# Optimization experiments

Hardware: AMD Instinct MI355X
Metric: run time of the kernel (lower is better)

## Reference

```python
import jax, jax.numpy as jnp
import numpy as np

B, H, W = 8, 56, 56
DIM, DIM_OUT, NUM_HEADS = 96, 192, 3
Q_STRIDE = (2, 2)


def setup_inputs() -> dict:
    key = jax.random.key(0)
    k1, k2, k3 = jax.random.split(key, 3)
    x = jax.random.normal(k1, (B, H, W, DIM), dtype=jnp.float32)
    W_qkv = jax.random.normal(k2, (DIM, 3 * DIM_OUT), dtype=jnp.float32) * 0.02
    b_qkv = jnp.zeros((3 * DIM_OUT,), dtype=jnp.float32)
    W_proj = jax.random.normal(k3, (DIM_OUT, DIM_OUT), dtype=jnp.float32) * 0.02
    b_proj = jnp.zeros((DIM_OUT,), dtype=jnp.float32)
    return {"x": x, "W_qkv": W_qkv, "b_qkv": b_qkv, "W_proj": W_proj, "b_proj": b_proj}


def reference(x, W_qkv, b_qkv, W_proj, b_proj):
    b, h, w, _ = x.shape
    c = W_proj.shape[0]          # dim_out
    nh = NUM_HEADS
    hd = c // nh                 # head_dim
    sh, sw = Q_STRIDE

    # fused QKV projection: (B,H,W,3*C)
    qkv = jnp.einsum("bhwd,de->bhwe", x, W_qkv) + b_qkv
    qkv = qkv.reshape(b, h * w, 3, nh, hd)
    q, k, v = qkv[:, :, 0], qkv[:, :, 1], qkv[:, :, 2]  # each (B,N,nh,hd)

    # query max-pool over spatial dims (channels = nh*hd, heads interleaved as in original)
    q = q.reshape(b, h, w, c)
    q = q.reshape(b, h // sh, sh, w // sw, sw, c).max(axis=(2, 4))  # (B,H',W',C)
    hn, wn = h // sh, w // sw
    q = q.reshape(b, hn * wn, nh, hd)

    # heads-first layout, scaled q
    q = q.transpose(0, 2, 1, 3) / jnp.sqrt(jnp.asarray(hd, x.dtype))  # (B,nh,Nq,hd)
    k = k.transpose(0, 2, 1, 3)                                       # (B,nh,Nk,hd)
    v = v.transpose(0, 2, 1, 3)

    attn = jax.nn.softmax(jnp.einsum("bnqd,bnkd->bnqk", q, k), axis=-1)
    out = jnp.einsum("bnqk,bnkd->bnqd", attn, v)        # (B,nh,Nq,hd)
    out = out.transpose(0, 2, 1, 3).reshape(b, hn, wn, c)

    return jnp.einsum("bhwc,cd->bhwd", out, W_proj) + b_proj
```

## Files before the change

### kernel.cpp

```cpp
#include <hip/hip_runtime.h>

#define BB    8
#define DIMO  192
#define NH    3
#define HD    64
#define NK    3136
#define NQ    784
#define M1    25088
#define M2    6272
#define KSPLIT 7
#define KSLICE 448
#define PSTR  56

#define QSCALE 0.18033688011112042f

#if __has_builtin(__builtin_amdgcn_mfma_f32_16x16x16bf16_1k)
#define HAVE_MFMA16 1
#else
#define HAVE_MFMA16 0
#endif

#if __has_builtin(__builtin_amdgcn_exp2f)
#define FEXP2(x) __builtin_amdgcn_exp2f(x)
#else
#define FEXP2(x) exp2f(x)
#endif

typedef __bf16 bf16x8 __attribute__((ext_vector_type(8)));
typedef float f32x4  __attribute__((ext_vector_type(4)));
typedef short s16x4  __attribute__((ext_vector_type(4)));

__device__ inline unsigned short f2bf(float f) {
    unsigned int u = __builtin_bit_cast(unsigned int, f);
    u += 0x7FFFu + ((u >> 16) & 1u);
    return (unsigned short)(u >> 16);
}

__device__ inline unsigned int pk_bf16(float a, float b) {
    unsigned int ua = __builtin_bit_cast(unsigned int, a) + 0x8000u;
    unsigned int ub = __builtin_bit_cast(unsigned int, b) + 0x8000u;
    return __builtin_amdgcn_perm(ub, ua, 0x07060302u);
}

__global__ void wprep(const float* __restrict__ Wqkv, const float* __restrict__ Wproj,
                      unsigned short* __restrict__ Wb, unsigned short* __restrict__ Wpb) {
    __shared__ float Ls[192][33];
    const int t = threadIdx.x;
    if (blockIdx.x < 18) {
        const int n0 = blockIdx.x * 32;
        int rr = t >> 5, c = t & 31;
#pragma unroll
        for (int rb = 0; rb < 12; ++rb) {
            int row = rb * 8 + rr;
            Ls[row][c] = Wqkv[(size_t)row * 576 + n0 + c];
        }
        __syncthreads();
        int n = t >> 3, kc = (t & 7) * 12;
#pragma unroll
        for (int j = 0; j < 12; j += 4) {
            ushort4 u = { f2bf(Ls[kc + j][n]), f2bf(Ls[kc + j + 1][n]),
                          f2bf(Ls[kc + j + 2][n]), f2bf(Ls[kc + j + 3][n]) };
            *(ushort4*)(Wb + (size_t)(n0 + n) * 96 + kc + j) = u;
        }
    } else {
        const int n0 = (blockIdx.x - 18) * 32;
        int rr = t >> 5, c = t & 31;
#pragma unroll
        for (int rb = 0; rb < 24; ++rb) {
            int row = rb * 8 + rr;
            Ls[row][c] = Wproj[(size_t)row * 192 + n0 + c];
        }
        __syncthreads();
        int n = t >> 3, kc = (t & 7) * 24;
#pragma unroll
        for (int j = 0; j < 24; j += 4) {
            ushort4 u = { f2bf(Ls[kc + j][n]), f2bf(Ls[kc + j + 1][n]),
                          f2bf(Ls[kc + j + 2][n]), f2bf(Ls[kc + j + 3][n]) };
            *(ushort4*)(Wpb + (size_t)(n0 + n) * 192 + kc + j) = u;
        }
    }
}

__launch_bounds__(256)
__global__ void qkv_fused(const float* __restrict__ x,
                          const unsigned short* __restrict__ Wb,
                          const float* __restrict__ bias,
                          unsigned short* __restrict__ Qpb,
                          unsigned short* __restrict__ Kb,
                          unsigned short* __restrict__ Vt) {
    __shared__ __attribute__((aligned(16))) unsigned short xs[112 * 104];
    const int tid = threadIdx.x;
    const int wave = tid >> 6, lane = tid & 63;
    const int quad = lane >> 4, l16 = lane & 15;
    const int bid = blockIdx.x;

    if (bid < 392) {
        const int m0 = bid * 64;
#pragma unroll
        for (int i = 0; i < 6; ++i) {
            int f = tid + i * 256;
            int r = f / 24, c4 = f % 24;
            float4 v = ((const float4*)x)[(size_t)(m0 + r) * 24 + c4];
            ushort4 u = { f2bf(v.x), f2bf(v.y), f2bf(v.z), f2bf(v.w) };
            *(ushort4*)&xs[r * 104 + c4 * 4] = u;
        }
        __syncthreads();

        const int mbase = m0 + wave * 16 + quad * 4;
        const int b = m0 / NK;
        const int key = mbase - b * NK;

#pragma unroll
        for (int sec = 1; sec <= 2; ++sec) {
            f32x4 acc[12];
#pragma unroll
            for (int i = 0; i < 12; ++i) acc[i] = (f32x4){0.f, 0.f, 0.f, 0.f};

            const unsigned short* wb = Wb + (size_t)(sec * 192 + l16) * 96 + quad * 8;
#pragma unroll
            for (int ch = 0; ch < 3; ++ch) {
                bf16x8 af = *(const bf16x8*)&xs[(wave * 16 + l16) * 104 + ch * 32 + quad * 8];
#pragma unroll
                for (int nf = 0; nf < 12; ++nf) {
                    bf16x8 bfr = *(const bf16x8*)(wb + (size_t)nf * 16 * 96 + ch * 32);
                    acc[nf] = __builtin_amdgcn_mfma_f32_16x16x32_bf16(af, bfr, acc[nf], 0, 0, 0);
                }
            }

            if (sec == 1) {
#pragma unroll
                for (int nf = 0; nf < 12; ++nf) {
                    int n = nf * 16 + l16;
                    float bs = bias[192 + n];
#pragma unroll
                    for (int i = 0; i < 4; ++i)
                        Kb[(size_t)(mbase + i) * 192 + n] = f2bf(acc[nf][i] + bs);
                }
            } else {
#pragma unroll
                for (int nf = 0; nf < 12; ++nf) {
                    int n = nf * 16 + l16;
                    float bs = bias[384 + n];
                    int hh = n >> 6, dd = n & 63;
                    ushort4 u = { f2bf(acc[nf][0] + bs), f2bf(acc[nf][1] + bs),
                                  f2bf(acc[nf][2] + bs), f2bf(acc[nf][3] + bs) };
                    *(ushort4*)(Vt + ((size_t)((b * 3 + hh) * 64 + dd)) * NK + key) = u;
                }
            }
        }
    } else {
        const int t = bid - 392;
        const int b = t / 28, hq = t % 28;
        const int m0 = b * NK + hq * 112;
#pragma unroll
        for (int i = 0; i < 11; ++i) {
            int f = tid + i * 256;
            if (f < 2688) {
                int r = f / 24, c4 = f % 24;
                float4 v = ((const float4*)x)[(size_t)(m0 + r) * 24 + c4];
                int rp = 2 * (r % 56) + (r / 56);
                ushort4 u = { f2bf(v.x), f2bf(v.y), f2bf(v.z), f2bf(v.w) };
                *(ushort4*)&xs[rp * 104 + c4 * 4] = u;
            }
        }
        __syncthreads();

        f32x4 acc[7][3];
#pragma unroll
        for (int i = 0; i < 7; ++i)
#pragma unroll
            for (int j = 0; j < 3; ++j) acc[i][j] = (f32x4){0.f, 0.f, 0.f, 0.f};

        const unsigned short* wb = Wb + (size_t)(wave * 48 + l16) * 96 + quad * 8;
#pragma unroll
        for (int ch = 0; ch < 3; ++ch) {
            bf16x8 bfr[3];
#pragma unroll
            for (int jf = 0; jf < 3; ++jf)
                bfr[jf] = *(const bf16x8*)(wb + (size_t)jf * 16 * 96 + ch * 32);
#pragma unroll
            for (int mf = 0; mf < 7; ++mf) {
                bf16x8 a = *(const bf16x8*)&xs[(mf * 16 + l16) * 104 + ch * 32 + quad * 8];
#pragma unroll
                for (int jf = 0; jf < 3; ++jf)
                    acc[mf][jf] = __builtin_amdgcn_mfma_f32_16x16x32_bf16(a, bfr[jf], acc[mf][jf], 0, 0, 0);
            }
        }

#pragma unroll
        for (int mf = 0; mf < 7; ++mf) {
            int q = hq * 28 + mf * 4 + quad;
#pragma unroll
            for (int jf = 0; jf < 3; ++jf) {
                int n = wave * 48 + jf * 16 + l16;
                float m = fmaxf(fmaxf(acc[mf][jf][0], acc[mf][jf][1]),
                                fmaxf(acc[mf][jf][2], acc[mf][jf][3]));
                m = (m + bias[n]) * QSCALE;
                int hh = n >> 6, dd = n & 63;
                Qpb[((size_t)(b * 3 + hh) * NQ + q) * 64 + dd] = f2bf(m);
            }
        }
    }
}

__launch_bounds__(256)
__global__ void attn_mfma(const unsigned short* __restrict__ Qpb,
                          const unsigned short* __restrict__ Kb,
                          const unsigned short* __restrict__ Vt,
                          float* __restrict__ Pnum,
                          float* __restrict__ Pden) {
    __shared__ __attribute__((aligned(16))) unsigned short Ks[64 * 88];
    __shared__ __attribute__((aligned(16))) unsigned short Vs[64 * 88];
#if !HAVE_MFMA16
    __shared__ __attribute__((aligned(16))) unsigned short Ps[4 * 32 * PSTR];
#endif

    const int tid = threadIdx.x;
    const int wave = tid >> 6, lane = tid & 63;
    const int quad = lane >> 4, l16 = lane & 15;
    const int bh = blockIdx.y, b = bh / NH, h = bh % NH;
    const int qt = blockIdx.x * 128 + wave * 32;
    const int ks = blockIdx.z, k00 = ks * KSLICE;

    const int srow0 = tid >> 3, sch = (tid & 7) * 8;
    const unsigned short* kg  = Kb + ((size_t)(b * NK + k00) + srow0) * DIMO + h * 64 + sch;
    const unsigned short* kg1 = kg + (size_t)32 * DIMO;
    const unsigned short* vg  = Vt + ((size_t)bh * 64 + srow0) * NK + k00 + sch;
    const unsigned short* vg1 = vg + (size_t)32 * NK;

    uint4 kp0 = *(const uint4*)kg;
    uint4 kp1 = *(const uint4*)kg1;
    uint4 vp0 = *(const uint4*)vg;
    uint4 vp1 = *(const uint4*)vg1;

    int qa = min(qt + l16, NQ - 1);
    int qb = min(qt + 16 + l16, NQ - 1);
    const unsigned short* qpa = Qpb + ((size_t)bh * NQ + qa) * HD + quad * 8;
    const unsigned short* qpc = Qpb + ((size_t)bh * NQ + qb) * HD + quad * 8;
    bf16x8 qf[2][2];
    qf[0][0] = *(const bf16x8*)qpa;  qf[0][1] = *(const bf16x8*)(qpa + 32);
    qf[1][0] = *(const bf16x8*)qpc;  qf[1][1] = *(const bf16x8*)(qpc + 32);

    f32x4 on[4][2];
#pragma unroll
    for (int i = 0; i < 4; ++i)
#pragma unroll
        for (int j = 0; j < 2; ++j) on[i][j] = (f32x4){0.f, 0.f, 0.f, 0.f};
    f32x4 dn[2];
    dn[0] = (f32x4){0.f, 0.f, 0.f, 0.f};
    dn[1] = (f32x4){0.f, 0.f, 0.f, 0.f};

#if HAVE_MFMA16
    const short one16 = (short)0x3F80;
    s16x4 ones4 = { one16, one16, one16, one16 };
#else
    const __bf16 one = (__bf16)1.0f;
    bf16x8 ones8 = { one, one, one, one, one, one, one, one };
    unsigned short* myP = Ps + wave * 32 * PSTR;
#endif

    for (int s = 0; s < 7; ++s) {
        __syncthreads();
        *(uint4*)&Ks[srow0 * 88 + sch]        = kp0;
        *(uint4*)&Ks[(srow0 + 32) * 88 + sch] = kp1;
        *(uint4*)&Vs[srow0 * 88 + sch]        = vp0;
        *(uint4*)&Vs[(srow0 + 32) * 88 + sch] = vp1;
        __syncthreads();
        if (s < 6) {
            kp0 = *(const uint4*)(kg  + (size_t)(s + 1) * 64 * DIMO);
            kp1 = *(const uint4*)(kg1 + (size_t)(s + 1) * 64 * DIMO);
            vp0 = *(const uint4*)(vg  + (s + 1) * 64);
            vp1 = *(const uint4*)(vg1 + (s + 1) * 64);
        }

#if HAVE_MFMA16
#pragma unroll
        for (int g = 0; g < 4; ++g) {
            const int krow = (g * 16 + l16) * 88;
            bf16x8 kf0 = *(const bf16x8*)&Ks[krow + quad * 8];
            bf16x8 kf1 = *(const bf16x8*)&Ks[krow + 32 + quad * 8];
            s16x4 vf[4];
#pragma unroll
            for (int dsub = 0; dsub < 4; ++dsub)
                vf[dsub] = *(const s16x4*)&Vs[(dsub * 16 + l16) * 88 + g * 16 + quad * 4];
#pragma unroll
            for (int qsub = 0; qsub < 2; ++qsub) {
                f32x4 sa = (f32x4){0.f, 0.f, 0.f, 0.f};
                sa = __builtin_amdgcn_mfma_f32_16x16x32_bf16(kf0, qf[qsub][0], sa, 0, 0, 0);
                sa = __builtin_amdgcn_mfma_f32_16x16x32_bf16(kf1, qf[qsub][1], sa, 0, 0, 0);
                float p0 = FEXP2(sa[0]), p1 = FEXP2(sa[1]);
                float p2 = FEXP2(sa[2]), p3 = FEXP2(sa[3]);
                uint2 pk = { pk_bf16(p0, p1), pk_bf16(p2, p3) };
                s16x4 pb = __builtin_bit_cast(s16x4, pk);
                dn[qsub] = __builtin_amdgcn_mfma_f32_16x16x16bf16_1k(ones4, pb, dn[qsub], 0, 0, 0);
#pragma unroll
                for (int dsub = 0; dsub < 4; ++dsub)
                    on[dsub][qsub] = __builtin_amdgcn_mfma_f32_16x16x16bf16_1k(
                        vf[dsub], pb, on[dsub][qsub], 0, 0, 0);
            }
        }
#else
#pragma unroll
        for (int half = 0; half < 2; ++half) {
#pragma unroll
            for (int ksub = 0; ksub < 2; ++ksub) {
                const int krow = (half * 32 + ksub * 16 + l16) * 88;
                bf16x8 kf0 = *(const bf16x8*)&Ks[krow + quad * 8];
                bf16x8 kf1 = *(const bf16x8*)&Ks[krow + 32 + quad * 8];
#pragma unroll
                for (int qsub = 0; qsub < 2; ++qsub) {
                    f32x4 sa = (f32x4){0.f, 0.f, 0.f, 0.f};
                    sa = __builtin_amdgcn_mfma_f32_16x16x32_bf16(kf0, qf[qsub][0], sa, 0, 0, 0);
                    sa = __builtin_amdgcn_mfma_f32_16x16x32_bf16(kf1, qf[qsub][1], sa, 0, 0, 0);
                    float p0 = FEXP2(sa[0]), p1 = FEXP2(sa[1]);
                    float p2 = FEXP2(sa[2]), p3 = FEXP2(sa[3]);
                    uint2 pk = { pk_bf16(p0, p1), pk_bf16(p2, p3) };
                    *(uint2*)&myP[(qsub * 16 + l16) * PSTR + ksub * 16 + quad * 4] = pk;
                }
            }
            bf16x8 pf0 = *(const bf16x8*)&myP[l16 * PSTR + quad * 8];
            bf16x8 pf1 = *(const bf16x8*)&myP[(16 + l16) * PSTR + quad * 8];
            dn[0] = __builtin_amdgcn_mfma_f32_16x16x32_bf16(ones8, pf0, dn[0], 0, 0, 0);
            dn[1] = __builtin_amdgcn_mfma_f32_16x16x32_bf16(ones8, pf1, dn[1], 0, 0, 0);
#pragma unroll
            for (int dsub = 0; dsub < 4; ++dsub) {
                bf16x8 vf = *(const bf16x8*)&Vs[(dsub * 16 + l16) * 88 + half * 32 + quad * 8];
                on[dsub][0] = __builtin_amdgcn_mfma_f32_16x16x32_bf16(vf, pf0, on[dsub][0], 0, 0, 0);
                on[dsub][1] = __builtin_amdgcn_mfma_f32_16x16x32_bf16(vf, pf1, on[dsub][1], 0, 0, 0);
            }
        }
#endif
    }

#pragma unroll
    for (int qsub = 0; qsub < 2; ++qsub) {
        int q = qt + qsub * 16 + l16;
        if (q < NQ) {
            size_t base = (size_t)ks * (24 * NQ * HD) + ((size_t)bh * NQ + q) * HD + quad * 4;
#pragma unroll
            for (int dsub = 0; dsub < 4; ++dsub)
                *(f32x4*)(Pnum + base + dsub * 16) = on[dsub][qsub];
            if (quad == 0) Pden[ks * (24 * NQ) + bh * NQ + q] = dn[qsub][0];
        }
    }
}

__launch_bounds__(256)
__global__ void proj_comb(const float* __restrict__ Pnum,
                          const float* __restrict__ Pden,
                          const unsigned short* __restrict__ Wpb,
                          const float* __restrict__ bproj,
                          float* __restrict__ out) {
    __shared__ __attribute__((aligned(16))) unsigned short as_[16 * 200];
    __shared__ float rden[16][4];
    const int tid = threadIdx.x;
    const int wave = tid >> 6, lane = tid & 63;
    const int quad = lane >> 4, l16 = lane & 15;
    const int m0 = blockIdx.x * 16;

    if (tid < 48) {
        int r = tid / 3, h = tid % 3;
        int gq = m0 + r, b = gq / NQ, qq = gq - b * NQ;
        float den = 0.f;
#pragma unroll
        for (int s = 0; s < KSPLIT; ++s)
            den += Pden[s * (24 * NQ) + (b * 3 + h) * NQ + qq];
        rden[r][h] = 1.0f / den;
    }
    __syncthreads();

    {
        int r = tid >> 4, cl = tid & 15;
        int gq = m0 + r, b = gq / NQ, qq = gq - b * NQ;
#pragma unroll
        for (int i = 0; i < 3; ++i) {
            int c = cl + i * 16;
            int h = c >> 4, d = (c & 15) * 4;
            const float* p = Pnum + ((size_t)(b * 3 + h) * NQ + qq) * 64 + d;
            f32x4 num = (f32x4){0.f, 0.f, 0.f, 0.f};
#pragma unroll
            for (int s = 0; s < KSPLIT; ++s)
                num = num + *(const f32x4*)(p + (size_t)s * (24 * NQ * HD));
            float rc = rden[r][h];
            ushort4 u = { f2bf(num[0] * rc), f2bf(num[1] * rc),
                          f2bf(num[2] * rc), f2bf(num[3] * rc) };
            *(ushort4*)&as_[r * 200 + c * 4] = u;
        }
    }
    __syncthreads();

    f32x4 acc[3];
#pragma unroll
    for (int j = 0; j < 3; ++j) acc[j] = (f32x4){0.f, 0.f, 0.f, 0.f};

    const unsigned short* wp = Wpb + (size_t)(wave * 48 + l16) * 192 + quad * 8;
#pragma unroll
    for (int ch = 0; ch < 6; ++ch) {
        bf16x8 a = *(const bf16x8*)&as_[l16 * 200 + ch * 32 + quad * 8];
#pragma unroll
        for (int jf = 0; jf < 3; ++jf) {
            bf16x8 bfr = *(const bf16x8*)(wp + (size_t)jf * 16 * 192 + ch * 32);
            acc[jf] = __builtin_amdgcn_mfma_f32_16x16x32_bf16(a, bfr, acc[jf], 0, 0, 0);
        }
    }

    const int m = m0 + quad * 4;
#pragma unroll
    for (int jf = 0; jf < 3; ++jf) {
        int n = wave * 48 + jf * 16 + l16;
        float bs = bproj[n];
#pragma unroll
        for (int i = 0; i < 4; ++i)
            out[(size_t)(m + i) * 192 + n] = acc[jf][i] + bs;
    }
}

extern "C" void kernel_launch(void* const* d_in, const int* in_sizes, int n_in,
                              void* d_out, int out_size, void* d_ws, size_t ws_size,
                              hipStream_t stream) {
    const float* x     = (const float*)d_in[0];
    const float* Wqkv  = (const float*)d_in[1];
    const float* bqkv  = (const float*)d_in[2];
    const float* Wproj = (const float*)d_in[3];
    const float* bproj = (const float*)d_in[4];
    float* out = (float*)d_out;

    float* Pnum = (float*)d_ws;
    float* Pden = Pnum + (size_t)KSPLIT * 24 * NQ * HD;
    unsigned short* Qpb = (unsigned short*)(Pden + (size_t)KSPLIT * 24 * NQ);
    unsigned short* Kb  = Qpb + (size_t)24 * NQ * HD;
    unsigned short* Vt  = Kb + (size_t)BB * NK * DIMO;
    unsigned short* Wb  = Vt + (size_t)24 * HD * NK;
    unsigned short* Wpb = Wb + (size_t)576 * 96;

    wprep<<<24, 256, 0, stream>>>(Wqkv, Wproj, Wb, Wpb);

    qkv_fused<<<616, 256, 0, stream>>>(x, Wb, bqkv, Qpb, Kb, Vt);

    attn_mfma<<<dim3(7, 24, KSPLIT), 256, 0, stream>>>(Qpb, Kb, Vt, Pnum, Pden);

    proj_comb<<<392, 256, 0, stream>>>(Pnum, Pden, Wpb, bproj, out);
}
```

Baseline: 138.4 us.

## Split K/V blocks, remap attention grid per XCD, store partial numerators as bf16

```diff
diff --git a/kernel.cpp b/kernel.cpp
--- a/kernel.cpp
+++ b/kernel.cpp
@@ -34,6 +34,11 @@
     unsigned int u = __builtin_bit_cast(unsigned int, f);
     u += 0x7FFFu + ((u >> 16) & 1u);
     return (unsigned short)(u >> 16);
+}
+
+__device__ inline float bf2f(unsigned short u) {
+    unsigned int x = (unsigned int)u << 16;
+    return __builtin_bit_cast(float, x);
 }
 
 __device__ inline unsigned int pk_bf16(float a, float b) {
@@ -94,8 +99,9 @@
     const int quad = lane >> 4, l16 = lane & 15;
     const int bid = blockIdx.x;
 
-    if (bid < 392) {
-        const int m0 = bid * 64;
+    if (bid < 784) {
+        const int sec = (bid < 392) ? 1 : 2;
+        const int m0 = ((bid < 392) ? bid : bid - 392) * 64;
 #pragma unroll
         for (int i = 0; i < 6; ++i) {
             int f = tid + i * 256;
@@ -106,50 +112,46 @@
         }
         __syncthreads();
 
+        f32x4 acc[12];
+#pragma unroll
+        for (int i = 0; i < 12; ++i) acc[i] = (f32x4){0.f, 0.f, 0.f, 0.f};
+
+        const unsigned short* wb = Wb + (size_t)(sec * 192 + l16) * 96 + quad * 8;
+#pragma unroll
+        for (int ch = 0; ch < 3; ++ch) {
+            bf16x8 af = *(const bf16x8*)&xs[(wave * 16 + l16) * 104 + ch * 32 + quad * 8];
+#pragma unroll
+            for (int nf = 0; nf < 12; ++nf) {
+                bf16x8 bfr = *(const bf16x8*)(wb + (size_t)nf * 16 * 96 + ch * 32);
+                acc[nf] = __builtin_amdgcn_mfma_f32_16x16x32_bf16(af, bfr, acc[nf], 0, 0, 0);
+            }
+        }
+
         const int mbase = m0 + wave * 16 + quad * 4;
-        const int b = m0 / NK;
-        const int key = mbase - b * NK;
-
-#pragma unroll
-        for (int sec = 1; sec <= 2; ++sec) {
-            f32x4 acc[12];
-#pragma unroll
-            for (int i = 0; i < 12; ++i) acc[i] = (f32x4){0.f, 0.f, 0.f, 0.f};
-
-            const unsigned short* wb = Wb + (size_t)(sec * 192 + l16) * 96 + quad * 8;
-#pragma unroll
-            for (int ch = 0; ch < 3; ++ch) {
-                bf16x8 af = *(const bf16x8*)&xs[(wave * 16 + l16) * 104 + ch * 32 + quad * 8];
-#pragma unroll
-                for (int nf = 0; nf < 12; ++nf) {
-                    bf16x8 bfr = *(const bf16x8*)(wb + (size_t)nf * 16 * 96 + ch * 32);
-                    acc[nf] = __builtin_amdgcn_mfma_f32_16x16x32_bf16(af, bfr, acc[nf], 0, 0, 0);
-                }
-            }
-
-            if (sec == 1) {
-#pragma unroll
-                for (int nf = 0; nf < 12; ++nf) {
-                    int n = nf * 16 + l16;
-                    float bs = bias[192 + n];
-#pragma unroll
-                    for (int i = 0; i < 4; ++i)
-                        Kb[(size_t)(mbase + i) * 192 + n] = f2bf(acc[nf][i] + bs);
-                }
-            } else {
-#pragma unroll
-                for (int nf = 0; nf < 12; ++nf) {
-                    int n = nf * 16 + l16;
-                    float bs = bias[384 + n];
-                    int hh = n >> 6, dd = n & 63;
-                    ushort4 u = { f2bf(acc[nf][0] + bs), f2bf(acc[nf][1] + bs),
-                                  f2bf(acc[nf][2] + bs), f2bf(acc[nf][3] + bs) };
-                    *(ushort4*)(Vt + ((size_t)((b * 3 + hh) * 64 + dd)) * NK + key) = u;
-                }
+        if (sec == 1) {
+#pragma unroll
+            for (int nf = 0; nf < 12; ++nf) {
+                int n = nf * 16 + l16;
+                float bs = bias[192 + n];
+#pragma unroll
+                for (int i = 0; i < 4; ++i)
+                    Kb[(size_t)(mbase + i) * 192 + n] = f2bf(acc[nf][i] + bs);
+            }
+        } else {
+            int b = m0 / NK;
+            int key = mbase - b * NK;
+#pragma unroll
+            for (int nf = 0; nf < 12; ++nf) {
+                int n = nf * 16 + l16;
+                float bs = bias[384 + n];
+                int hh = n >> 6, dd = n & 63;
+                ushort4 u = { f2bf(acc[nf][0] + bs), f2bf(acc[nf][1] + bs),
+                              f2bf(acc[nf][2] + bs), f2bf(acc[nf][3] + bs) };
+                *(ushort4*)(Vt + ((size_t)((b * 3 + hh) * 64 + dd)) * NK + key) = u;
             }
         }
     } else {
-        const int t = bid - 392;
+        const int t = bid - 784;
         const int b = t / 28, hq = t % 28;
         const int m0 = b * NK + hq * 112;
 #pragma unroll
@@ -207,7 +209,7 @@
 __global__ void attn_mfma(const unsigned short* __restrict__ Qpb,
                           const unsigned short* __restrict__ Kb,
                           const unsigned short* __restrict__ Vt,
-                          float* __restrict__ Pnum,
+                          unsigned short* __restrict__ Pnum,
                           float* __restrict__ Pden) {
     __shared__ __attribute__((aligned(16))) unsigned short Ks[64 * 88];
     __shared__ __attribute__((aligned(16))) unsigned short Vs[64 * 88];
@@ -218,9 +220,16 @@
     const int tid = threadIdx.x;
     const int wave = tid >> 6, lane = tid & 63;
     const int quad = lane >> 4, l16 = lane & 15;
-    const int bh = blockIdx.y, b = bh / NH, h = bh % NH;
-    const int qt = blockIdx.x * 128 + wave * 32;
-    const int ks = blockIdx.z, k00 = ks * KSLICE;
+
+    const int bid = blockIdx.x;
+    const int xcd = bid & 7, slot = bid >> 3;
+    const int bh = xcd * 3 + slot / 49;
+    const int inner = slot % 49;
+    const int qt = (inner / 7) * 128 + wave * 32;
+    const int ks = inner % 7;
+
+    const int b = bh / NH, h = bh % NH;
+    const int k00 = ks * KSLICE;
 
     const int srow0 = tid >> 3, sch = (tid & 7) * 8;
     const unsigned short* kg  = Kb + ((size_t)(b * NK + k00) + srow0) * DIMO + h * 64 + sch;
@@ -338,15 +347,18 @@
         if (q < NQ) {
             size_t base = (size_t)ks * (24 * NQ * HD) + ((size_t)bh * NQ + q) * HD + quad * 4;
 #pragma unroll
-            for (int dsub = 0; dsub < 4; ++dsub)
-                *(f32x4*)(Pnum + base + dsub * 16) = on[dsub][qsub];
+            for (int dsub = 0; dsub < 4; ++dsub) {
+                uint2 pk = { pk_bf16(on[dsub][qsub][0], on[dsub][qsub][1]),
+                             pk_bf16(on[dsub][qsub][2], on[dsub][qsub][3]) };
+                *(uint2*)(Pnum + base + dsub * 16) = pk;
+            }
             if (quad == 0) Pden[ks * (24 * NQ) + bh * NQ + q] = dn[qsub][0];
         }
     }
 }
 
 __launch_bounds__(256)
-__global__ void proj_comb(const float* __restrict__ Pnum,
+__global__ void proj_comb(const unsigned short* __restrict__ Pnum,
                           const float* __restrict__ Pden,
                           const unsigned short* __restrict__ Wpb,
                           const float* __restrict__ bproj,
@@ -356,31 +368,35 @@
     const int tid = threadIdx.x;
     const int wave = tid >> 6, lane = tid & 63;
     const int quad = lane >> 4, l16 = lane & 15;
-    const int m0 = blockIdx.x * 16;
+    const int bb_ = blockIdx.x & 7;
+    const int m0 = bb_ * NQ + (blockIdx.x >> 3) * 16;
 
     if (tid < 48) {
         int r = tid / 3, h = tid % 3;
-        int gq = m0 + r, b = gq / NQ, qq = gq - b * NQ;
+        int qq = m0 + r - bb_ * NQ;
         float den = 0.f;
 #pragma unroll
         for (int s = 0; s < KSPLIT; ++s)
-            den += Pden[s * (24 * NQ) + (b * 3 + h) * NQ + qq];
+            den += Pden[s * (24 * NQ) + (bb_ * 3 + h) * NQ + qq];
         rden[r][h] = 1.0f / den;
     }
     __syncthreads();
 
     {
         int r = tid >> 4, cl = tid & 15;
-        int gq = m0 + r, b = gq / NQ, qq = gq - b * NQ;
+        int qq = m0 + r - bb_ * NQ;
 #pragma unroll
         for (int i = 0; i < 3; ++i) {
             int c = cl + i * 16;
             int h = c >> 4, d = (c & 15) * 4;
-            const float* p = Pnum + ((size_t)(b * 3 + h) * NQ + qq) * 64 + d;
+            const unsigned short* p = Pnum + ((size_t)(bb_ * 3 + h) * NQ + qq) * 64 + d;
             f32x4 num = (f32x4){0.f, 0.f, 0.f, 0.f};
 #pragma unroll
-            for (int s = 0; s < KSPLIT; ++s)
-                num = num + *(const f32x4*)(p + (size_t)s * (24 * NQ * HD));
+            for (int s = 0; s < KSPLIT; ++s) {
+                ushort4 u4 = *(const ushort4*)(p + (size_t)s * (24 * NQ * HD));
+                num[0] += bf2f(u4.x); num[1] += bf2f(u4.y);
+                num[2] += bf2f(u4.z); num[3] += bf2f(u4.w);
+            }
             float rc = rden[r][h];
             ushort4 u = { f2bf(num[0] * rc), f2bf(num[1] * rc),
                           f2bf(num[2] * rc), f2bf(num[3] * rc) };
@@ -425,8 +441,8 @@
     const float* bproj = (const float*)d_in[4];
     float* out = (float*)d_out;
 
-    float* Pnum = (float*)d_ws;
-    float* Pden = Pnum + (size_t)KSPLIT * 24 * NQ * HD;
+    unsigned short* Pnum = (unsigned short*)d_ws;
+    float* Pden = (float*)(Pnum + (size_t)KSPLIT * 24 * NQ * HD);
     unsigned short* Qpb = (unsigned short*)(Pden + (size_t)KSPLIT * 24 * NQ);
     unsigned short* Kb  = Qpb + (size_t)24 * NQ * HD;
     unsigned short* Vt  = Kb + (size_t)BB * NK * DIMO;
@@ -435,9 +451,9 @@
 
     wprep<<<24, 256, 0, stream>>>(Wqkv, Wproj, Wb, Wpb);
 
-    qkv_fused<<<616, 256, 0, stream>>>(x, Wb, bqkv, Qpb, Kb, Vt);
-
-    attn_mfma<<<dim3(7, 24, KSPLIT), 256, 0, stream>>>(Qpb, Kb, Vt, Pnum, Pden);
+    qkv_fused<<<1008, 256, 0, stream>>>(x, Wb, bqkv, Qpb, Kb, Vt);
+
+    attn_mfma<<<1176, 256, 0, stream>>>(Qpb, Kb, Vt, Pnum, Pden);
 
     proj_comb<<<392, 256, 0, stream>>>(Pnum, Pden, Wpb, bproj, out);
 }
```

Result: faster. 125.6 us (-9.2%).
